# Kernel optimization log

Hardware: AMD Instinct MI355X
Metric: run time of the kernel (lower is better)

## Reference

```python
import jax, jax.numpy as jnp
import numpy as np

DIM = 2048
SEQ = 8192
NUM_HEADS = 16
PROJ_DIM = DIM // 4  # proj_ratio = 4.0
EPS = 1e-5


def setup_inputs() -> dict:
    key = jax.random.key(0)
    ks = jax.random.split(key, 8)
    s = 0.02  # param init scale
    return {
        "x": jax.random.normal(ks[0], (SEQ, DIM), jnp.float32),
        "q": jax.random.normal(ks[1], (1, DIM), jnp.float32),
        "W_kv": jax.random.normal(ks[2], (2 * DIM, DIM), jnp.float32) * s,
        "b_kv": jax.random.normal(ks[3], (2 * DIM,), jnp.float32) * s,
        "W_p1": jax.random.normal(ks[4], (PROJ_DIM, DIM), jnp.float32) * s,
        "b_p1": jax.random.normal(ks[5], (PROJ_DIM,), jnp.float32) * s,
        "W_p2": jax.random.normal(ks[6], (DIM, PROJ_DIM), jnp.float32) * s,
        "b_p2": jax.random.normal(ks[7], (DIM,), jnp.float32) * s,
        "ln_w": jnp.ones((PROJ_DIM,), jnp.float32),
        "ln_b": jnp.zeros((PROJ_DIM,), jnp.float32),
    }


def reference(x, q, W_kv, b_kv, W_p1, b_p1, W_p2, b_p2, ln_w, ln_b):
    seq, dim = x.shape
    h = NUM_HEADS
    d = dim // h

    # kv projection: [s, 2*dim]; split '(n h d)' with n leading -> k = first dim cols
    kv = x @ W_kv.T + b_kv
    k = kv[:, :dim].reshape(seq, h, d).transpose(1, 0, 2)   # [h, s, d]
    v = kv[:, dim:].reshape(seq, h, d).transpose(1, 0, 2)   # [h, s, d]
    qh = q.reshape(h, 1, d)                                  # '1 (h d) -> h 1 d'

    # single-query attention (qk_norm=False -> Identity norms)
    attn = jnp.einsum('hqd,hkd->hqk', qh, k) / jnp.sqrt(jnp.asarray(d, x.dtype))
    attn = jax.nn.softmax(attn, axis=-1)                     # [h, 1, s]
    x1 = jnp.einsum('hqk,hkd->hqd', attn, v)                 # [h, 1, d]
    x1 = x1.transpose(1, 0, 2).reshape(1, dim)               # 'h s d -> s (h d)'

    # proj MLP: proj1 -> LayerNorm -> relu -> proj2
    h1 = x1 @ W_p1.T + b_p1                                  # [1, proj_dim]
    mu = jnp.mean(h1, axis=-1, keepdims=True)
    var = jnp.mean(jnp.square(h1 - mu), axis=-1, keepdims=True)
    h1 = (h1 - mu) / jnp.sqrt(var + EPS) * ln_w + ln_b
    x1 = jax.nn.relu(h1) @ W_p2.T + b_p2                     # [1, dim]

    # residual broadcast: [s, dim] + [1, dim]
    return x + x1
```

## Files before the change

kernel.cpp:

```cpp
#include <hip/hip_runtime.h>
#include <math.h>

#define SEQ   8192
#define DIM   2048
#define NH    16
#define DH    128
#define PD    512

static constexpr float LN_EPS = 1e-5f;
static constexpr float SCALE  = 0.08838834764831845f;

typedef __bf16 bf16x8 __attribute__((ext_vector_type(8)));
typedef float  f32x4  __attribute__((ext_vector_type(4)));

static constexpr size_t OFF_QB   = 0;
static constexpr size_t OFF_SMP  = 16;
static constexpr size_t OFF_QWB  = 528;
static constexpr size_t OFF_ELOG = OFF_QWB + 16384;
static constexpr size_t OFF_PCTX = OFF_ELOG + 131072;
static constexpr size_t OFF_CTX  = OFF_PCTX + 128*32768;
static constexpr size_t OFF_X1   = OFF_CTX + 32768;
static constexpr size_t OFF_H1R  = OFF_X1 + 2048;
static constexpr size_t OFF_X1F  = OFF_H1R + 512;

__global__ __launch_bounds__(256) void k_prep(const float* __restrict__ q,
                                              const float* __restrict__ Wkv,
                                              const float* __restrict__ bkv,
                                              __bf16* __restrict__ qWb,
                                              float* __restrict__ qb,
                                              float* __restrict__ smp) {
    int t = threadIdx.x;
    int h = blockIdx.x >> 4, jc = blockIdx.x & 15;
    int col = t & 127, kh = t >> 7;
    int j = jc * 128 + col;
    const float* w  = Wkv + (size_t)(h * DH + kh * 64) * DIM + j;
    const float* qh = q + h * DH + kh * 64;
    float acc = 0.f;
#pragma unroll 16
    for (int d = 0; d < 64; ++d)
        acc += qh[d] * w[(size_t)d * DIM];
    __shared__ float part[128];
    if (kh) part[col] = acc;
    __syncthreads();
    if (!kh) qWb[h * DIM + j] = (__bf16)(acc + part[col]);
    if (jc == 0 && t < 64) {
        float p = q[h*DH + t] * bkv[h*DH + t] + q[h*DH + 64 + t] * bkv[h*DH + 64 + t];
        for (int off = 32; off; off >>= 1) p += __shfl_down(p, off);
        if (t == 0) qb[h] = p;
    }
    if (blockIdx.x == 0) { smp[t] = 0.f; smp[t + 256] = 0.f; }
}

__global__ __launch_bounds__(256) void k_logits(const float* __restrict__ x,
                                                const __bf16* __restrict__ qWb,
                                                const float* __restrict__ qb,
                                                float* __restrict__ elogT,
                                                float* __restrict__ smp) {
    const int t = threadIdx.x;
    const int w = t >> 6, lane = t & 63;
    const int r = lane & 15, quad = lane >> 4;
    const int s0 = blockIdx.x * 16;
    __shared__ float dpart[4][64][4];
    __shared__ float hsum[NH];
    if (t < NH) hsum[t] = 0.f;

    const float*  xrow = x + (size_t)(s0 + r) * DIM + quad * 8;
    const __bf16* brow = qWb + r * DIM + quad * 8;
    const int kbase = w * 512;

    f32x4 acc = {0.f, 0.f, 0.f, 0.f};
#pragma unroll 4
    for (int i = 0; i < 16; ++i) {
        int k = kbase + i * 32;
        float4 xa = *(const float4*)(xrow + k);
        float4 xb = *(const float4*)(xrow + k + 4);
        bf16x8 af;
        af[0] = (__bf16)xa.x; af[1] = (__bf16)xa.y;
        af[2] = (__bf16)xa.z; af[3] = (__bf16)xa.w;
        af[4] = (__bf16)xb.x; af[5] = (__bf16)xb.y;
        af[6] = (__bf16)xb.z; af[7] = (__bf16)xb.w;
        bf16x8 bf = *(const bf16x8*)(brow + k);
        acc = __builtin_amdgcn_mfma_f32_16x16x32_bf16(af, bf, acc, 0, 0, 0);
    }
    dpart[w][lane][0] = acc[0];
    dpart[w][lane][1] = acc[1];
    dpart[w][lane][2] = acc[2];
    dpart[w][lane][3] = acc[3];
    __syncthreads();

    {
        const int lane2 = t & 63, reg = t >> 6;
        const int h = lane2 & 15, sl = (lane2 >> 4) * 4 + reg;
        float v = dpart[0][lane2][reg] + dpart[1][lane2][reg]
                + dpart[2][lane2][reg] + dpart[3][lane2][reg];
        float e = __expf((v + qb[h]) * SCALE);
        elogT[(size_t)(s0 + sl) * NH + h] = e;
        atomicAdd(&hsum[h], e);
    }
    __syncthreads();
    if (t < NH) atomicAdd(&smp[t * 32 + (blockIdx.x & 31)], hsum[t]);
}

__global__ __launch_bounds__(256) void k_ctx(const float* __restrict__ x,
                                             const float* __restrict__ elogT,
                                             const float* __restrict__ smp,
                                             float* __restrict__ pctx) {
    int jc = blockIdx.x & 3, sc = blockIdx.x >> 2, t = threadIdx.x;
    int s0 = sc * 64;
    int j = jc * 512 + t * 2;
    __shared__ float inv_s[NH];
    __shared__ float att[64][NH];
    if (t < NH) {
        float S = 0.f;
#pragma unroll
        for (int i = 0; i < 32; ++i) S += smp[t * 32 + i];
        inv_s[t] = 1.0f / S;
    }
    __syncthreads();
    for (int i = t; i < 64 * NH; i += 256) {
        int rr = i >> 4, h = i & 15;
        att[rr][h] = elogT[(size_t)(s0 + rr) * NH + h] * inv_s[h];
    }
    __syncthreads();
    float2 acc[NH];
#pragma unroll
    for (int h = 0; h < NH; ++h) acc[h] = make_float2(0.f, 0.f);
    for (int rr = 0; rr < 64; ++rr) {
        float2 xv = *(const float2*)&x[(size_t)(s0 + rr) * DIM + j];
        const float4* ar = (const float4*)att[rr];
        float4 a0 = ar[0], a1 = ar[1], a2 = ar[2], a3 = ar[3];
        float aa[NH];
        *(float4*)&aa[0] = a0; *(float4*)&aa[4]  = a1;
        *(float4*)&aa[8] = a2; *(float4*)&aa[12] = a3;
#pragma unroll
        for (int h = 0; h < NH; ++h) {
            acc[h].x += aa[h] * xv.x;
            acc[h].y += aa[h] * xv.y;
        }
    }
#pragma unroll
    for (int h = 0; h < NH; ++h)
        *(float2*)&pctx[((size_t)(sc * NH + h)) * DIM + j] = acc[h];
}

__global__ __launch_bounds__(256) void k_ctxred(const float* __restrict__ pctx,
                                                float* __restrict__ ctx) {
    int idx = blockIdx.x * 256 + threadIdx.x;
    float s = 0.f;
#pragma unroll 8
    for (int sc = 0; sc < 128; ++sc)
        s += pctx[(size_t)sc * (NH * DIM) + idx];
    ctx[idx] = s;
}

__global__ __launch_bounds__(256) void k_x1(const float* __restrict__ Wkv,
                                            const float* __restrict__ bkv,
                                            const float* __restrict__ ctx,
                                            float* __restrict__ x1) {
    int row = blockIdx.x * 4 + (threadIdx.x >> 6);
    int lane = threadIdx.x & 63;
    const float* w = Wkv + (size_t)(DIM + row) * DIM;
    const float* c = ctx + (row >> 7) * DIM;
    float acc = 0.f;
#pragma unroll
    for (int k = 0; k < 8; ++k) {
        int j = k * 256 + lane * 4;
        float4 wv = *(const float4*)&w[j];
        float4 cv = *(const float4*)&c[j];
        acc += wv.x*cv.x + wv.y*cv.y + wv.z*cv.z + wv.w*cv.w;
    }
    for (int off = 32; off; off >>= 1) acc += __shfl_xor(acc, off);
    if (lane == 0) x1[row] = acc + bkv[DIM + row];
}

__global__ __launch_bounds__(256) void k_h1(const float* __restrict__ Wp1,
                                            const float* __restrict__ bp1,
                                            const float* __restrict__ x1,
                                            float* __restrict__ h1raw) {
    int row = blockIdx.x * 4 + (threadIdx.x >> 6);
    int lane = threadIdx.x & 63;
    const float* w = Wp1 + (size_t)row * DIM;
    float acc = 0.f;
#pragma unroll
    for (int k = 0; k < 8; ++k) {
        int j = k * 256 + lane * 4;
        float4 wv = *(const float4*)&w[j];
        float4 cv = *(const float4*)&x1[j];
        acc += wv.x*cv.x + wv.y*cv.y + wv.z*cv.z + wv.w*cv.w;
    }
    for (int off = 32; off; off >>= 1) acc += __shfl_xor(acc, off);
    if (lane == 0) h1raw[row] = acc + bp1[row];
}

__global__ __launch_bounds__(256) void k_x1f(const float* __restrict__ Wp2,
                                             const float* __restrict__ bp2,
                                             const float* __restrict__ h1raw,
                                             const float* __restrict__ lnw,
                                             const float* __restrict__ lnb,
                                             float* __restrict__ x1f) {
    int row = blockIdx.x * 4 + (threadIdx.x >> 6);
    int lane = threadIdx.x & 63;
    int j = lane * 8;
    float4 va = *(const float4*)&h1raw[j];
    float4 vb = *(const float4*)&h1raw[j + 4];
    float s = va.x + va.y + va.z + va.w + vb.x + vb.y + vb.z + vb.w;
    for (int off = 32; off; off >>= 1) s += __shfl_xor(s, off);
    float mu = s * (1.0f / PD);
    float dx[8];
    dx[0]=va.x-mu; dx[1]=va.y-mu; dx[2]=va.z-mu; dx[3]=va.w-mu;
    dx[4]=vb.x-mu; dx[5]=vb.y-mu; dx[6]=vb.z-mu; dx[7]=vb.w-mu;
    float s2 = 0.f;
#pragma unroll
    for (int i = 0; i < 8; ++i) s2 += dx[i] * dx[i];
    for (int off = 32; off; off >>= 1) s2 += __shfl_xor(s2, off);
    float rstd = rsqrtf(s2 * (1.0f / PD) + LN_EPS);
    float4 lw0 = *(const float4*)&lnw[j], lw1 = *(const float4*)&lnw[j + 4];
    float4 lb0 = *(const float4*)&lnb[j], lb1 = *(const float4*)&lnb[j + 4];
    float hln[8];
    hln[0]=fmaxf(dx[0]*rstd*lw0.x+lb0.x,0.f); hln[1]=fmaxf(dx[1]*rstd*lw0.y+lb0.y,0.f);
    hln[2]=fmaxf(dx[2]*rstd*lw0.z+lb0.z,0.f); hln[3]=fmaxf(dx[3]*rstd*lw0.w+lb0.w,0.f);
    hln[4]=fmaxf(dx[4]*rstd*lw1.x+lb1.x,0.f); hln[5]=fmaxf(dx[5]*rstd*lw1.y+lb1.y,0.f);
    hln[6]=fmaxf(dx[6]*rstd*lw1.z+lb1.z,0.f); hln[7]=fmaxf(dx[7]*rstd*lw1.w+lb1.w,0.f);
    const float* w = Wp2 + (size_t)row * PD + j;
    float4 w0 = *(const float4*)w, w1 = *(const float4*)(w + 4);
    float acc = w0.x*hln[0] + w0.y*hln[1] + w0.z*hln[2] + w0.w*hln[3]
              + w1.x*hln[4] + w1.y*hln[5] + w1.z*hln[6] + w1.w*hln[7];
    for (int off = 32; off; off >>= 1) acc += __shfl_xor(acc, off);
    if (lane == 0) x1f[row] = acc + bp2[row];
}

__global__ __launch_bounds__(256) void k_out(const float* __restrict__ x,
                                             const float* __restrict__ x1f,
                                             float* __restrict__ out) {
    size_t i = (size_t)blockIdx.x * 512 + threadIdx.x;
    float4 xv = ((const float4*)x)[i];
    float4 a  = ((const float4*)x1f)[(int)(i & 511)];
    ((float4*)out)[i] = make_float4(xv.x + a.x, xv.y + a.y, xv.z + a.z, xv.w + a.w);
    size_t i2 = i + 256;
    float4 xv2 = ((const float4*)x)[i2];
    float4 a2  = ((const float4*)x1f)[(int)(i2 & 511)];
    ((float4*)out)[i2] = make_float4(xv2.x + a2.x, xv2.y + a2.y, xv2.z + a2.z, xv2.w + a2.w);
}

extern "C" void kernel_launch(void* const* d_in, const int* in_sizes, int n_in,
                              void* d_out, int out_size, void* d_ws, size_t ws_size,
                              hipStream_t stream) {
    const float* x    = (const float*)d_in[0];
    const float* q    = (const float*)d_in[1];
    const float* Wkv  = (const float*)d_in[2];
    const float* bkv  = (const float*)d_in[3];
    const float* Wp1  = (const float*)d_in[4];
    const float* bp1  = (const float*)d_in[5];
    const float* Wp2  = (const float*)d_in[6];
    const float* bp2  = (const float*)d_in[7];
    const float* lnw  = (const float*)d_in[8];
    const float* lnb  = (const float*)d_in[9];
    float* out = (float*)d_out;
    float* ws  = (float*)d_ws;

    float*  qb    = ws + OFF_QB;
    float*  smp   = ws + OFF_SMP;
    __bf16* qWb   = (__bf16*)(ws + OFF_QWB);
    float*  elogT = ws + OFF_ELOG;
    float*  pctx  = ws + OFF_PCTX;
    float*  ctx   = ws + OFF_CTX;
    float*  x1    = ws + OFF_X1;
    float*  h1raw = ws + OFF_H1R;
    float*  x1f   = ws + OFF_X1F;

    k_prep  <<<256, 256, 0, stream>>>(q, Wkv, bkv, qWb, qb, smp);
    k_logits<<<512, 256, 0, stream>>>(x, qWb, qb, elogT, smp);
    k_ctx   <<<512, 256, 0, stream>>>(x, elogT, smp, pctx);
    k_ctxred<<<128, 256, 0, stream>>>(pctx, ctx);
    k_x1    <<<512, 256, 0, stream>>>(Wkv, bkv, ctx, x1);
    k_h1    <<<128, 256, 0, stream>>>(Wp1, bp1, x1, h1raw);
    k_x1f   <<<512, 256, 0, stream>>>(Wp2, bp2, h1raw, lnw, lnb, x1f);
    k_out   <<<8192, 256, 0, stream>>>(x, x1f, out);
}
```

Before: 223.7 us.

## Fuse all stages into one persistent kernel with software grid barriers

Replaces the eight-kernel pipeline with an init kernel and a single persistent 256-block kernel. Stages are separated by atomic-counter grid barriers, which removes launch gaps. The logits and context passes are fused so the exp weights stay in shared memory instead of going through a global buffer. Partial contexts now cover 32 rows per block, so the reduction has 256 partials, and softmax normalization is applied once after the reduction. The software barrier assumes all 256 blocks are co-resident and has a bounded spin, which risks a hang or wrong results if residency fails.

Result: slower. 315.1 us (+40.8%).

```diff
diff --git a/kernel.cpp b/kernel.cpp
--- a/kernel.cpp
+++ b/kernel.cpp
@@ -6,6 +6,8 @@
 #define NH    16
 #define DH    128
 #define PD    512
+#define NBLK  256
+#define NTHR  512
 
 static constexpr float LN_EPS = 1e-5f;
 static constexpr float SCALE  = 0.08838834764831845f;
@@ -16,230 +18,251 @@
 static constexpr size_t OFF_QB   = 0;
 static constexpr size_t OFF_SMP  = 16;
 static constexpr size_t OFF_QWB  = 528;
-static constexpr size_t OFF_ELOG = OFF_QWB + 16384;
-static constexpr size_t OFF_PCTX = OFF_ELOG + 131072;
-static constexpr size_t OFF_CTX  = OFF_PCTX + 128*32768;
+static constexpr size_t OFF_PCTX = 16912;
+static constexpr size_t OFF_CTX  = OFF_PCTX + 8388608;
 static constexpr size_t OFF_X1   = OFF_CTX + 32768;
 static constexpr size_t OFF_H1R  = OFF_X1 + 2048;
 static constexpr size_t OFF_X1F  = OFF_H1R + 512;
-
-__global__ __launch_bounds__(256) void k_prep(const float* __restrict__ q,
-                                              const float* __restrict__ Wkv,
-                                              const float* __restrict__ bkv,
-                                              __bf16* __restrict__ qWb,
-                                              float* __restrict__ qb,
-                                              float* __restrict__ smp) {
-    int t = threadIdx.x;
-    int h = blockIdx.x >> 4, jc = blockIdx.x & 15;
-    int col = t & 127, kh = t >> 7;
-    int j = jc * 128 + col;
-    const float* w  = Wkv + (size_t)(h * DH + kh * 64) * DIM + j;
-    const float* qh = q + h * DH + kh * 64;
-    float acc = 0.f;
-#pragma unroll 16
-    for (int d = 0; d < 64; ++d)
-        acc += qh[d] * w[(size_t)d * DIM];
-    __shared__ float part[128];
-    if (kh) part[col] = acc;
+static constexpr size_t OFF_BAR  = OFF_X1F + 2048;
+
+__device__ __forceinline__ void gsync(unsigned int* bar) {
     __syncthreads();
-    if (!kh) qWb[h * DIM + j] = (__bf16)(acc + part[col]);
-    if (jc == 0 && t < 64) {
-        float p = q[h*DH + t] * bkv[h*DH + t] + q[h*DH + 64 + t] * bkv[h*DH + 64 + t];
-        for (int off = 32; off; off >>= 1) p += __shfl_down(p, off);
-        if (t == 0) qb[h] = p;
-    }
-    if (blockIdx.x == 0) { smp[t] = 0.f; smp[t + 256] = 0.f; }
-}
-
-__global__ __launch_bounds__(256) void k_logits(const float* __restrict__ x,
-                                                const __bf16* __restrict__ qWb,
-                                                const float* __restrict__ qb,
-                                                float* __restrict__ elogT,
-                                                float* __restrict__ smp) {
-    const int t = threadIdx.x;
-    const int w = t >> 6, lane = t & 63;
-    const int r = lane & 15, quad = lane >> 4;
-    const int s0 = blockIdx.x * 16;
-    __shared__ float dpart[4][64][4];
+    if (threadIdx.x == 0) {
+        __threadfence();
+        atomicAdd(bar, 1u);
+        for (unsigned int it = 0; it < (1u << 21); ++it) {
+            unsigned int v = __hip_atomic_load(bar, __ATOMIC_ACQUIRE,
+                                               __HIP_MEMORY_SCOPE_AGENT);
+            if (v >= (unsigned int)NBLK) break;
+            __builtin_amdgcn_s_sleep(2);
+        }
+    }
+    __syncthreads();
+}
+
+__global__ __launch_bounds__(512) void k_init(float* smp, unsigned int* bars) {
+    smp[threadIdx.x] = 0.f;
+    if (threadIdx.x < 8) bars[threadIdx.x] = 0u;
+}
+
+__global__ __launch_bounds__(NTHR, 2) void k_mega(
+    const float* __restrict__ x,   const float* __restrict__ q,
+    const float* __restrict__ Wkv, const float* __restrict__ bkv,
+    const float* __restrict__ Wp1, const float* __restrict__ bp1,
+    const float* __restrict__ Wp2, const float* __restrict__ bp2,
+    const float* __restrict__ lnw, const float* __restrict__ lnb,
+    float* __restrict__ out, float* __restrict__ ws)
+{
+    const int b = blockIdx.x, t = threadIdx.x;
+    const int w8 = t >> 6, lane = t & 63;
+
+    float*        qb    = ws + OFF_QB;
+    float*        smp   = ws + OFF_SMP;
+    __bf16*       qWb   = (__bf16*)(ws + OFF_QWB);
+    float*        pctx  = ws + OFF_PCTX;
+    float*        ctx   = ws + OFF_CTX;
+    float*        x1    = ws + OFF_X1;
+    float*        h1raw = ws + OFF_H1R;
+    float*        x1f   = ws + OFF_X1F;
+    unsigned int* bars  = (unsigned int*)(ws + OFF_BAR);
+
+    __shared__ float part[4][128];
+    __shared__ float qred[8];
+    __shared__ float dpart[2][4][64][4];
+    __shared__ float att[32][NH];
     __shared__ float hsum[NH];
-    if (t < NH) hsum[t] = 0.f;
-
-    const float*  xrow = x + (size_t)(s0 + r) * DIM + quad * 8;
-    const __bf16* brow = qWb + r * DIM + quad * 8;
-    const int kbase = w * 512;
-
-    f32x4 acc = {0.f, 0.f, 0.f, 0.f};
+    __shared__ float psum[4][128];
+    __shared__ float sInv;
+
+    {
+        const int h = b >> 4, jc = b & 15;
+        const int col = t & 127, kh = t >> 7;
+        const int j = jc * 128 + col;
+        const float* w  = Wkv + (size_t)(h * DH + kh * 32) * DIM + j;
+        const float* qh = q + h * DH + kh * 32;
+        float acc = 0.f;
+#pragma unroll
+        for (int d = 0; d < 32; ++d)
+            acc += qh[d] * w[(size_t)d * DIM];
+        part[kh][col] = acc;
+        __syncthreads();
+        if (kh == 0)
+            qWb[h * DIM + j] = (__bf16)(part[0][col] + part[1][col]
+                                      + part[2][col] + part[3][col]);
+        if (jc == 0) {
+            float p = (t < DH) ? q[h * DH + t] * bkv[h * DH + t] : 0.f;
+            for (int off = 32; off; off >>= 1) p += __shfl_xor(p, off);
+            if (lane == 0) qred[w8] = p;
+            __syncthreads();
+            if (t == 0) {
+                float s = 0.f;
+#pragma unroll
+                for (int i = 0; i < 8; ++i) s += qred[i];
+                qb[h] = s;
+            }
+        }
+    }
+    gsync(bars + 0);
+
+    {
+        const int s0 = b * 32;
+        const int rg = w8 & 1, kq = w8 >> 1;
+        const int r = lane & 15, quad = lane >> 4;
+        if (t < NH) hsum[t] = 0.f;
+
+        const float*  xrow = x + (size_t)(s0 + rg * 16 + r) * DIM + quad * 8;
+        const __bf16* brow = qWb + r * DIM + quad * 8;
+        const int kbase = kq * 512;
+        f32x4 acc = {0.f, 0.f, 0.f, 0.f};
 #pragma unroll 4
-    for (int i = 0; i < 16; ++i) {
-        int k = kbase + i * 32;
-        float4 xa = *(const float4*)(xrow + k);
-        float4 xb = *(const float4*)(xrow + k + 4);
-        bf16x8 af;
-        af[0] = (__bf16)xa.x; af[1] = (__bf16)xa.y;
-        af[2] = (__bf16)xa.z; af[3] = (__bf16)xa.w;
-        af[4] = (__bf16)xb.x; af[5] = (__bf16)xb.y;
-        af[6] = (__bf16)xb.z; af[7] = (__bf16)xb.w;
-        bf16x8 bf = *(const bf16x8*)(brow + k);
-        acc = __builtin_amdgcn_mfma_f32_16x16x32_bf16(af, bf, acc, 0, 0, 0);
-    }
-    dpart[w][lane][0] = acc[0];
-    dpart[w][lane][1] = acc[1];
-    dpart[w][lane][2] = acc[2];
-    dpart[w][lane][3] = acc[3];
-    __syncthreads();
-
-    {
-        const int lane2 = t & 63, reg = t >> 6;
-        const int h = lane2 & 15, sl = (lane2 >> 4) * 4 + reg;
-        float v = dpart[0][lane2][reg] + dpart[1][lane2][reg]
-                + dpart[2][lane2][reg] + dpart[3][lane2][reg];
-        float e = __expf((v + qb[h]) * SCALE);
-        elogT[(size_t)(s0 + sl) * NH + h] = e;
-        atomicAdd(&hsum[h], e);
-    }
-    __syncthreads();
-    if (t < NH) atomicAdd(&smp[t * 32 + (blockIdx.x & 31)], hsum[t]);
-}
-
-__global__ __launch_bounds__(256) void k_ctx(const float* __restrict__ x,
-                                             const float* __restrict__ elogT,
-                                             const float* __restrict__ smp,
-                                             float* __restrict__ pctx) {
-    int jc = blockIdx.x & 3, sc = blockIdx.x >> 2, t = threadIdx.x;
-    int s0 = sc * 64;
-    int j = jc * 512 + t * 2;
-    __shared__ float inv_s[NH];
-    __shared__ float att[64][NH];
-    if (t < NH) {
-        float S = 0.f;
-#pragma unroll
-        for (int i = 0; i < 32; ++i) S += smp[t * 32 + i];
-        inv_s[t] = 1.0f / S;
-    }
-    __syncthreads();
-    for (int i = t; i < 64 * NH; i += 256) {
-        int rr = i >> 4, h = i & 15;
-        att[rr][h] = elogT[(size_t)(s0 + rr) * NH + h] * inv_s[h];
-    }
-    __syncthreads();
-    float2 acc[NH];
-#pragma unroll
-    for (int h = 0; h < NH; ++h) acc[h] = make_float2(0.f, 0.f);
-    for (int rr = 0; rr < 64; ++rr) {
-        float2 xv = *(const float2*)&x[(size_t)(s0 + rr) * DIM + j];
-        const float4* ar = (const float4*)att[rr];
-        float4 a0 = ar[0], a1 = ar[1], a2 = ar[2], a3 = ar[3];
-        float aa[NH];
-        *(float4*)&aa[0] = a0; *(float4*)&aa[4]  = a1;
-        *(float4*)&aa[8] = a2; *(float4*)&aa[12] = a3;
-#pragma unroll
-        for (int h = 0; h < NH; ++h) {
-            acc[h].x += aa[h] * xv.x;
-            acc[h].y += aa[h] * xv.y;
-        }
-    }
-#pragma unroll
-    for (int h = 0; h < NH; ++h)
-        *(float2*)&pctx[((size_t)(sc * NH + h)) * DIM + j] = acc[h];
-}
-
-__global__ __launch_bounds__(256) void k_ctxred(const float* __restrict__ pctx,
-                                                float* __restrict__ ctx) {
-    int idx = blockIdx.x * 256 + threadIdx.x;
-    float s = 0.f;
+        for (int i = 0; i < 16; ++i) {
+            int k = kbase + i * 32;
+            float4 xa  = *(const float4*)(xrow + k);
+            float4 xb2 = *(const float4*)(xrow + k + 4);
+            bf16x8 af;
+            af[0] = (__bf16)xa.x;  af[1] = (__bf16)xa.y;
+            af[2] = (__bf16)xa.z;  af[3] = (__bf16)xa.w;
+            af[4] = (__bf16)xb2.x; af[5] = (__bf16)xb2.y;
+            af[6] = (__bf16)xb2.z; af[7] = (__bf16)xb2.w;
+            bf16x8 bfv = *(const bf16x8*)(brow + k);
+            acc = __builtin_amdgcn_mfma_f32_16x16x32_bf16(af, bfv, acc, 0, 0, 0);
+        }
+        *(f32x4*)&dpart[rg][kq][lane][0] = acc;
+        __syncthreads();
+
+        {
+            const int h = t & 15, slp = t >> 4;
+            const int rg2 = slp >> 4, sli = slp & 15;
+            const int quad2 = sli >> 2, reg2 = sli & 3;
+            const int lane2 = quad2 * 16 + h;
+            float v = dpart[rg2][0][lane2][reg2] + dpart[rg2][1][lane2][reg2]
+                    + dpart[rg2][2][lane2][reg2] + dpart[rg2][3][lane2][reg2];
+            float e = __expf((v + qb[h]) * SCALE);
+            att[slp][h] = e;
+            atomicAdd(&hsum[h], e);
+        }
+        __syncthreads();
+        if (t < NH) atomicAdd(&smp[t * 32 + (b & 31)], hsum[t]);
+
+        const int j0 = t * 4;
+        f32x4 zero = {0.f, 0.f, 0.f, 0.f};
+        f32x4 acc4[NH];
+#pragma unroll
+        for (int h = 0; h < NH; ++h) acc4[h] = zero;
+#pragma unroll 2
+        for (int rr = 0; rr < 32; ++rr) {
+            f32x4 xv = *(const f32x4*)(x + (size_t)(s0 + rr) * DIM + j0);
+            const f32x4* ar = (const f32x4*)att[rr];
+            f32x4 a0 = ar[0], a1 = ar[1], a2 = ar[2], a3 = ar[3];
+            float aa[16];
+            *(f32x4*)&aa[0] = a0; *(f32x4*)&aa[4]  = a1;
+            *(f32x4*)&aa[8] = a2; *(f32x4*)&aa[12] = a3;
+#pragma unroll
+            for (int h = 0; h < NH; ++h) acc4[h] += xv * aa[h];
+        }
+#pragma unroll
+        for (int h = 0; h < NH; ++h)
+            *(f32x4*)&pctx[((size_t)(b * NH + h)) * DIM + j0] = acc4[h];
+    }
+    gsync(bars + 1);
+
+    {
+        const int h = b >> 4;
+        float v = (t < 32) ? smp[h * 32 + t] : 0.f;
+        if (t < 64) {
+            for (int off = 16; off; off >>= 1) v += __shfl_xor(v, off);
+            if (t == 0) sInv = 1.f / v;
+        }
+        const int tg = t >> 7, tt = t & 127;
+        const size_t idx = (size_t)b * 128 + tt;
+        const int c0 = tg * 64;
+        float s = 0.f;
 #pragma unroll 8
-    for (int sc = 0; sc < 128; ++sc)
-        s += pctx[(size_t)sc * (NH * DIM) + idx];
-    ctx[idx] = s;
-}
-
-__global__ __launch_bounds__(256) void k_x1(const float* __restrict__ Wkv,
-                                            const float* __restrict__ bkv,
-                                            const float* __restrict__ ctx,
-                                            float* __restrict__ x1) {
-    int row = blockIdx.x * 4 + (threadIdx.x >> 6);
-    int lane = threadIdx.x & 63;
-    const float* w = Wkv + (size_t)(DIM + row) * DIM;
-    const float* c = ctx + (row >> 7) * DIM;
-    float acc = 0.f;
-#pragma unroll
-    for (int k = 0; k < 8; ++k) {
-        int j = k * 256 + lane * 4;
-        float4 wv = *(const float4*)&w[j];
-        float4 cv = *(const float4*)&c[j];
-        acc += wv.x*cv.x + wv.y*cv.y + wv.z*cv.z + wv.w*cv.w;
-    }
-    for (int off = 32; off; off >>= 1) acc += __shfl_xor(acc, off);
-    if (lane == 0) x1[row] = acc + bkv[DIM + row];
-}
-
-__global__ __launch_bounds__(256) void k_h1(const float* __restrict__ Wp1,
-                                            const float* __restrict__ bp1,
-                                            const float* __restrict__ x1,
-                                            float* __restrict__ h1raw) {
-    int row = blockIdx.x * 4 + (threadIdx.x >> 6);
-    int lane = threadIdx.x & 63;
-    const float* w = Wp1 + (size_t)row * DIM;
-    float acc = 0.f;
-#pragma unroll
-    for (int k = 0; k < 8; ++k) {
-        int j = k * 256 + lane * 4;
-        float4 wv = *(const float4*)&w[j];
-        float4 cv = *(const float4*)&x1[j];
-        acc += wv.x*cv.x + wv.y*cv.y + wv.z*cv.z + wv.w*cv.w;
-    }
-    for (int off = 32; off; off >>= 1) acc += __shfl_xor(acc, off);
-    if (lane == 0) h1raw[row] = acc + bp1[row];
-}
-
-__global__ __launch_bounds__(256) void k_x1f(const float* __restrict__ Wp2,
-                                             const float* __restrict__ bp2,
-                                             const float* __restrict__ h1raw,
-                                             const float* __restrict__ lnw,
-                                             const float* __restrict__ lnb,
-                                             float* __restrict__ x1f) {
-    int row = blockIdx.x * 4 + (threadIdx.x >> 6);
-    int lane = threadIdx.x & 63;
-    int j = lane * 8;
-    float4 va = *(const float4*)&h1raw[j];
-    float4 vb = *(const float4*)&h1raw[j + 4];
-    float s = va.x + va.y + va.z + va.w + vb.x + vb.y + vb.z + vb.w;
-    for (int off = 32; off; off >>= 1) s += __shfl_xor(s, off);
-    float mu = s * (1.0f / PD);
-    float dx[8];
-    dx[0]=va.x-mu; dx[1]=va.y-mu; dx[2]=va.z-mu; dx[3]=va.w-mu;
-    dx[4]=vb.x-mu; dx[5]=vb.y-mu; dx[6]=vb.z-mu; dx[7]=vb.w-mu;
-    float s2 = 0.f;
-#pragma unroll
-    for (int i = 0; i < 8; ++i) s2 += dx[i] * dx[i];
-    for (int off = 32; off; off >>= 1) s2 += __shfl_xor(s2, off);
-    float rstd = rsqrtf(s2 * (1.0f / PD) + LN_EPS);
-    float4 lw0 = *(const float4*)&lnw[j], lw1 = *(const float4*)&lnw[j + 4];
-    float4 lb0 = *(const float4*)&lnb[j], lb1 = *(const float4*)&lnb[j + 4];
-    float hln[8];
-    hln[0]=fmaxf(dx[0]*rstd*lw0.x+lb0.x,0.f); hln[1]=fmaxf(dx[1]*rstd*lw0.y+lb0.y,0.f);
-    hln[2]=fmaxf(dx[2]*rstd*lw0.z+lb0.z,0.f); hln[3]=fmaxf(dx[3]*rstd*lw0.w+lb0.w,0.f);
-    hln[4]=fmaxf(dx[4]*rstd*lw1.x+lb1.x,0.f); hln[5]=fmaxf(dx[5]*rstd*lw1.y+lb1.y,0.f);
-    hln[6]=fmaxf(dx[6]*rstd*lw1.z+lb1.z,0.f); hln[7]=fmaxf(dx[7]*rstd*lw1.w+lb1.w,0.f);
-    const float* w = Wp2 + (size_t)row * PD + j;
-    float4 w0 = *(const float4*)w, w1 = *(const float4*)(w + 4);
-    float acc = w0.x*hln[0] + w0.y*hln[1] + w0.z*hln[2] + w0.w*hln[3]
-              + w1.x*hln[4] + w1.y*hln[5] + w1.z*hln[6] + w1.w*hln[7];
-    for (int off = 32; off; off >>= 1) acc += __shfl_xor(acc, off);
-    if (lane == 0) x1f[row] = acc + bp2[row];
-}
-
-__global__ __launch_bounds__(256) void k_out(const float* __restrict__ x,
-                                             const float* __restrict__ x1f,
-                                             float* __restrict__ out) {
-    size_t i = (size_t)blockIdx.x * 512 + threadIdx.x;
-    float4 xv = ((const float4*)x)[i];
-    float4 a  = ((const float4*)x1f)[(int)(i & 511)];
-    ((float4*)out)[i] = make_float4(xv.x + a.x, xv.y + a.y, xv.z + a.z, xv.w + a.w);
-    size_t i2 = i + 256;
-    float4 xv2 = ((const float4*)x)[i2];
-    float4 a2  = ((const float4*)x1f)[(int)(i2 & 511)];
-    ((float4*)out)[i2] = make_float4(xv2.x + a2.x, xv2.y + a2.y, xv2.z + a2.z, xv2.w + a2.w);
+        for (int c = 0; c < 64; ++c)
+            s += pctx[(size_t)(c0 + c) * (NH * DIM) + idx];
+        psum[tg][tt] = s;
+        __syncthreads();
+        if (tg == 0)
+            ctx[idx] = (psum[0][tt] + psum[1][tt] + psum[2][tt] + psum[3][tt]) * sInv;
+    }
+    gsync(bars + 2);
+
+    {
+        const int row = b * 8 + w8;
+        const float* wv = Wkv + (size_t)(DIM + row) * DIM;
+        const float* cc = ctx + (size_t)(row >> 7) * DIM;
+        float acc = 0.f;
+#pragma unroll
+        for (int i = 0; i < 8; ++i) {
+            int j = i * 256 + lane * 4;
+            f32x4 a  = *(const f32x4*)(wv + j);
+            f32x4 c2 = *(const f32x4*)(cc + j);
+            acc += a[0]*c2[0] + a[1]*c2[1] + a[2]*c2[2] + a[3]*c2[3];
+        }
+        for (int off = 32; off; off >>= 1) acc += __shfl_xor(acc, off);
+        if (lane == 0) x1[row] = acc + bkv[DIM + row];
+    }
+    gsync(bars + 3);
+
+    if (w8 < 2) {
+        const int row = b * 2 + w8;
+        const float* wv = Wp1 + (size_t)row * DIM;
+        float acc = 0.f;
+#pragma unroll
+        for (int i = 0; i < 8; ++i) {
+            int j = i * 256 + lane * 4;
+            f32x4 a  = *(const f32x4*)(wv + j);
+            f32x4 c2 = *(const f32x4*)(x1 + j);
+            acc += a[0]*c2[0] + a[1]*c2[1] + a[2]*c2[2] + a[3]*c2[3];
+        }
+        for (int off = 32; off; off >>= 1) acc += __shfl_xor(acc, off);
+        if (lane == 0) h1raw[row] = acc + bp1[row];
+    }
+    gsync(bars + 4);
+
+    {
+        const int row = b * 8 + w8;
+        const int j = lane * 8;
+        f32x4 va  = *(const f32x4*)(h1raw + j);
+        f32x4 vb2 = *(const f32x4*)(h1raw + j + 4);
+        float s = va[0]+va[1]+va[2]+va[3]+vb2[0]+vb2[1]+vb2[2]+vb2[3];
+        for (int off = 32; off; off >>= 1) s += __shfl_xor(s, off);
+        float mu = s * (1.0f / PD);
+        float dx[8];
+        dx[0]=va[0]-mu;  dx[1]=va[1]-mu;  dx[2]=va[2]-mu;  dx[3]=va[3]-mu;
+        dx[4]=vb2[0]-mu; dx[5]=vb2[1]-mu; dx[6]=vb2[2]-mu; dx[7]=vb2[3]-mu;
+        float s2 = 0.f;
+#pragma unroll
+        for (int i = 0; i < 8; ++i) s2 += dx[i] * dx[i];
+        for (int off = 32; off; off >>= 1) s2 += __shfl_xor(s2, off);
+        float rstd = rsqrtf(s2 * (1.0f / PD) + LN_EPS);
+        f32x4 lw0 = *(const f32x4*)(lnw + j), lw1 = *(const f32x4*)(lnw + j + 4);
+        f32x4 lb0 = *(const f32x4*)(lnb + j), lb1 = *(const f32x4*)(lnb + j + 4);
+        float hln[8];
+        hln[0]=fmaxf(dx[0]*rstd*lw0[0]+lb0[0],0.f); hln[1]=fmaxf(dx[1]*rstd*lw0[1]+lb0[1],0.f);
+        hln[2]=fmaxf(dx[2]*rstd*lw0[2]+lb0[2],0.f); hln[3]=fmaxf(dx[3]*rstd*lw0[3]+lb0[3],0.f);
+        hln[4]=fmaxf(dx[4]*rstd*lw1[0]+lb1[0],0.f); hln[5]=fmaxf(dx[5]*rstd*lw1[1]+lb1[1],0.f);
+        hln[6]=fmaxf(dx[6]*rstd*lw1[2]+lb1[2],0.f); hln[7]=fmaxf(dx[7]*rstd*lw1[3]+lb1[3],0.f);
+        const float* w = Wp2 + (size_t)row * PD + j;
+        f32x4 w0 = *(const f32x4*)w, w1 = *(const f32x4*)(w + 4);
+        float acc = w0[0]*hln[0] + w0[1]*hln[1] + w0[2]*hln[2] + w0[3]*hln[3]
+                  + w1[0]*hln[4] + w1[1]*hln[5] + w1[2]*hln[6] + w1[3]*hln[7];
+        for (int off = 32; off; off >>= 1) acc += __shfl_xor(acc, off);
+        if (lane == 0) x1f[row] = acc + bp2[row];
+    }
+    gsync(bars + 5);
+
+    {
+        const f32x4* x4 = (const f32x4*)x;
+        f32x4*       o4 = (f32x4*)out;
+        const f32x4  add = ((const f32x4*)x1f)[t];
+        const size_t base = (size_t)b * NTHR + t;
+#pragma unroll 8
+        for (int k2 = 0; k2 < 32; ++k2) {
+            size_t i = (size_t)k2 * (NBLK * NTHR) + base;
+            o4[i] = x4[i] + add;
+        }
+    }
 }
 
 extern "C" void kernel_launch(void* const* d_in, const int* in_sizes, int n_in,
@@ -255,25 +278,9 @@
     const float* bp2  = (const float*)d_in[7];
     const float* lnw  = (const float*)d_in[8];
     const float* lnb  = (const float*)d_in[9];
-    float* out = (float*)d_out;
-    float* ws  = (float*)d_ws;
-
-    float*  qb    = ws + OFF_QB;
-    float*  smp   = ws + OFF_SMP;
-    __bf16* qWb   = (__bf16*)(ws + OFF_QWB);
-    float*  elogT = ws + OFF_ELOG;
-    float*  pctx  = ws + OFF_PCTX;
-    float*  ctx   = ws + OFF_CTX;
-    float*  x1    = ws + OFF_X1;
-    float*  h1raw = ws + OFF_H1R;
-    float*  x1f   = ws + OFF_X1F;
-
-    k_prep  <<<256, 256, 0, stream>>>(q, Wkv, bkv, qWb, qb, smp);
-    k_logits<<<512, 256, 0, stream>>>(x, qWb, qb, elogT, smp);
-    k_ctx   <<<512, 256, 0, stream>>>(x, elogT, smp, pctx);
-    k_ctxred<<<128, 256, 0, stream>>>(pctx, ctx);
-    k_x1    <<<512, 256, 0, stream>>>(Wkv, bkv, ctx, x1);
-    k_h1    <<<128, 256, 0, stream>>>(Wp1, bp1, x1, h1raw);
-    k_x1f   <<<512, 256, 0, stream>>>(Wp2, bp2, h1raw, lnw, lnb, x1f);
-    k_out   <<<8192, 256, 0, stream>>>(x, x1f, out);
-}
+    float* ws = (float*)d_ws;
+
+    k_init<<<1, 512, 0, stream>>>(ws + OFF_SMP, (unsigned int*)(ws + OFF_BAR));
+    k_mega<<<NBLK, NTHR, 0, stream>>>(x, q, Wkv, bkv, Wp1, bp1, Wp2, bp2,
+                                      lnw, lnb, (float*)d_out, ws);
+}
```
